# Kernel optimization log

Hardware: AMD Instinct MI355X
Metric: run time of the kernel (lower is better)

The kernel has to match this reference:

```python
import jax, jax.numpy as jnp
import numpy as np

N = 100000
E = 1600000
IN_DIM, HID, OUT = 128, 64, 16
NUM_CLASSES = 2
BN_EPS = 1e-5


def setup_inputs() -> dict:
    key = jax.random.key(0)
    ks = jax.random.split(key, 12)
    s = lambda fan_in: 1.0 / np.sqrt(fan_in)
    inp = {
        'x': jax.random.normal(ks[0], (N, IN_DIM), jnp.float32),
        'src': jax.random.randint(ks[1], (E,), 0, N, jnp.int32),
        'dst': jax.random.randint(ks[2], (E,), 0, N, jnp.int32),
        # SAGEConv1: lin_l (neighbors, bias) + lin_r (root, no bias)
        'W1l': jax.random.uniform(ks[3], (HID, IN_DIM), jnp.float32, -s(IN_DIM), s(IN_DIM)),
        'b1l': jnp.zeros((HID,), jnp.float32),
        'W1r': jax.random.uniform(ks[4], (HID, IN_DIM), jnp.float32, -s(IN_DIM), s(IN_DIM)),
        # BatchNorm1d(hidden)
        'gamma': jnp.ones((HID,), jnp.float32),
        'beta': jnp.zeros((HID,), jnp.float32),
        # SAGEConv2
        'W2l': jax.random.uniform(ks[5], (OUT, HID), jnp.float32, -s(HID), s(HID)),
        'b2l': jnp.zeros((OUT,), jnp.float32),
        'W2r': jax.random.uniform(ks[6], (OUT, HID), jnp.float32, -s(HID), s(HID)),
        # classifier Linear(emb_dim=16, 2)
        'Wc': jax.random.uniform(ks[7], (NUM_CLASSES, OUT), jnp.float32, -s(OUT), s(OUT)),
        'bc': jax.random.uniform(ks[8], (NUM_CLASSES,), jnp.float32, -s(OUT), s(OUT)),
    }
    return inp


def _sage_conv(x, src, dst, Wl, bl, Wr, deg_inv):
    # mean-aggregate neighbor features at dst, then linear; plus root transform
    agg = jax.ops.segment_sum(x[src], dst, num_segments=N) * deg_inv  # [N, F]
    return agg @ Wl.T + bl + x @ Wr.T


def _batchnorm_train(h, gamma, beta):
    mu = jnp.mean(h, axis=0)
    var = jnp.mean((h - mu) ** 2, axis=0)  # biased, as torch BN uses for normalization
    return (h - mu) * jax.lax.rsqrt(var + BN_EPS) * gamma + beta


def reference(x, src, dst, W1l, b1l, W1r, gamma, beta, W2l, b2l, W2r, Wc, bc):
    deg = jax.ops.segment_sum(jnp.ones((E,), x.dtype), dst, num_segments=N)
    deg_inv = (1.0 / jnp.maximum(deg, 1.0))[:, None]
    h = _sage_conv(x, src, dst, W1l, b1l, W1r, deg_inv)      # [N, HID]
    h = jax.nn.relu(_batchnorm_train(h, gamma, beta))
    emb = _sage_conv(h, src, dst, W2l, b2l, W2r, deg_inv)    # [N, OUT]
    logits = emb @ Wc.T + bc                                 # [N, 2]
    return (logits, emb)
```

## Files before the change

### kernel.cpp

```cpp
#include <hip/hip_runtime.h>

#define NN 100000
#define NB ((NN + 255) / 256)

__device__ __forceinline__ unsigned short f2bf(float x) {
    unsigned u = __float_as_uint(x);
    u += 0x7fff + ((u >> 16) & 1);
    return (unsigned short)(u >> 16);
}
__device__ __forceinline__ float bf2f(unsigned short h) {
    return __uint_as_float(((unsigned)h) << 16);
}

template<bool BF16>
__device__ __forceinline__ void gemm32x64(const float* __restrict__ x,
        const float* __restrict__ W, void* __restrict__ out,
        int rb, int tid, float (*lw)[68], float (*lx)[68]) {
    const int row0 = rb * 32;
    const int cg = tid & 15, rl = tid >> 4;
    float acc[2][4] = {{0.f,0.f,0.f,0.f},{0.f,0.f,0.f,0.f}};
    for (int kt = 0; kt < 2; ++kt) {
        if (kt) __syncthreads();
        for (int idx = tid; idx < 4096; idx += 256) {
            int j = idx >> 6, k = idx & 63;
            lw[k][j] = W[j * 128 + kt * 64 + k];
        }
        #pragma unroll
        for (int i = 0; i < 2; ++i) {
            int f4 = i * 256 + tid;
            int r = f4 >> 4, k4 = (f4 & 15) << 2;
            int grow = row0 + r;
            float4 vv = make_float4(0.f, 0.f, 0.f, 0.f);
            if (grow < NN) vv = *(const float4*)(x + (size_t)grow * 128 + kt * 64 + k4);
            *(float4*)(&lx[r][k4]) = vv;
        }
        __syncthreads();
        #pragma unroll
        for (int p = 0; p < 2; ++p) {
            int r = p * 16 + rl;
            #pragma unroll 8
            for (int k = 0; k < 64; ++k) {
                float xv = lx[r][k];
                float4 wv = *(const float4*)(&lw[k][cg << 2]);
                acc[p][0] = fmaf(xv, wv.x, acc[p][0]);
                acc[p][1] = fmaf(xv, wv.y, acc[p][1]);
                acc[p][2] = fmaf(xv, wv.z, acc[p][2]);
                acc[p][3] = fmaf(xv, wv.w, acc[p][3]);
            }
        }
    }
    #pragma unroll
    for (int p = 0; p < 2; ++p) {
        int grow = row0 + p * 16 + rl;
        if (grow < NN) {
            if (BF16) {
                ushort4 o;
                o.x = f2bf(acc[p][0]); o.y = f2bf(acc[p][1]);
                o.z = f2bf(acc[p][2]); o.w = f2bf(acc[p][3]);
                *(ushort4*)((unsigned short*)out + (size_t)grow * 64 + (cg << 2)) = o;
            } else {
                *(float4*)((float*)out + (size_t)grow * 64 + (cg << 2)) =
                    make_float4(acc[p][0], acc[p][1], acc[p][2], acc[p][3]);
            }
        }
    }
}

__global__ __launch_bounds__(256) void k_fusedA(const float* __restrict__ x,
        const float* __restrict__ W1l, const int* __restrict__ dst,
        int* __restrict__ deg, unsigned short* __restrict__ y1, int E) {
    __shared__ float lw[64][68];
    __shared__ float lx[32][68];
    const int tid = threadIdx.x;
    const int u = blockIdx.x >> 4, v = blockIdx.x & 15;
    if (v < 8) {
        const int base = (u * 8 + v) * 512;
        #pragma unroll
        for (int i = 0; i < 2; ++i) {
            int e = base + i * 256 + tid;
            if (e < E) atomicAdd(&deg[dst[e]], 1);
        }
        return;
    }
    const int rb = u * 8 + (v - 8);
    if (rb >= 3125) return;
    gemm32x64<true>(x, W1l, y1, rb, tid, lw, lx);
}

__global__ __launch_bounds__(256) void k_fusedB(const float* __restrict__ x,
        const float* __restrict__ W1r, const int* __restrict__ src,
        const int* __restrict__ dst, int* __restrict__ cursor,
        int* __restrict__ eidx, float* __restrict__ h, int E) {
    __shared__ float lw[64][68];
    __shared__ float lx[32][68];
    const int tid = threadIdx.x;
    const int u = blockIdx.x >> 4, v = blockIdx.x & 15;
    if (v < 8) {
        const int base = u * 4096;
        const int lo = v * 12500, hi = lo + 12500;
        #pragma unroll 4
        for (int i = 0; i < 16; ++i) {
            int e = base + i * 256 + tid;
            if (e < E) {
                int d = dst[e];
                if (d >= lo && d < hi) {
                    int pos = atomicAdd(&cursor[d], 1);
                    eidx[pos] = src[e];
                }
            }
        }
        return;
    }
    const int rb = u * 8 + (v - 8);
    if (rb >= 3125) return;
    gemm32x64<false>(x, W1r, h, rb, tid, lw, lx);
}

__global__ __launch_bounds__(256) void k_scanA(const int* __restrict__ deg,
                                               int* __restrict__ rowptr,
                                               int* __restrict__ bsum) {
    const int tid = threadIdx.x;
    const int i = blockIdx.x * 256 + tid;
    int v = (i < NN) ? deg[i] : 0;
    const int lane = tid & 63, w = tid >> 6;
    int inc = v;
    #pragma unroll
    for (int d = 1; d < 64; d <<= 1) {
        int t = __shfl_up(inc, d, 64);
        if (lane >= d) inc += t;
    }
    __shared__ int wsum[4];
    if (lane == 63) wsum[w] = inc;
    __syncthreads();
    int wo = 0;
    for (int k = 0; k < w; ++k) wo += wsum[k];
    if (i < NN) rowptr[i] = wo + inc - v;
    if (tid == 255) bsum[blockIdx.x] = wo + inc;
}

__global__ __launch_bounds__(512) void k_scanB(int* __restrict__ bsum,
                                               int* __restrict__ rowptr, int E) {
    const int tid = threadIdx.x;
    int v = (tid < NB) ? bsum[tid] : 0;
    const int lane = tid & 63, w = tid >> 6;
    int inc = v;
    #pragma unroll
    for (int d = 1; d < 64; d <<= 1) {
        int t = __shfl_up(inc, d, 64);
        if (lane >= d) inc += t;
    }
    __shared__ int wsum[8];
    if (lane == 63) wsum[w] = inc;
    __syncthreads();
    int wo = 0;
    for (int k = 0; k < w; ++k) wo += wsum[k];
    if (tid < NB) bsum[tid] = wo + inc - v;
    if (tid == 0) rowptr[NN] = E;
}

__global__ void k_finish(int* __restrict__ rowptr, const int* __restrict__ bsum,
                         const int* __restrict__ deg, int* __restrict__ cursor,
                         float* __restrict__ deg_inv) {
    int i = blockIdx.x * 256 + threadIdx.x;
    if (i < NN) {
        int rp = rowptr[i] + bsum[i >> 8];
        rowptr[i] = rp;
        cursor[i] = rp;
        deg_inv[i] = 1.0f / fmaxf((float)deg[i], 1.0f);
    }
}

__global__ __launch_bounds__(256) void k_gather1(const unsigned short* __restrict__ y1,
        const int* __restrict__ rowptr, const int* __restrict__ eidx,
        const float* __restrict__ b1l,
        const float* __restrict__ deg_inv, float* __restrict__ h,
        float* __restrict__ stats) {
    const int tid = threadIdx.x;
    const int f = tid & 63, w = tid >> 6;
    const float bias = b1l[f];
    float a1 = 0.f, a2 = 0.f;
    for (int n = blockIdx.x * 4 + w; n < NN; n += gridDim.x * 4) {
        int beg = rowptr[n], end = rowptr[n + 1];
        float s0 = 0.f, s1 = 0.f, s2 = 0.f, s3 = 0.f;
        int j = beg;
        for (; j + 3 < end; j += 4) {
            int i0 = eidx[j], i1 = eidx[j + 1], i2 = eidx[j + 2], i3 = eidx[j + 3];
            s0 += bf2f(y1[(size_t)i0 * 64 + f]);
            s1 += bf2f(y1[(size_t)i1 * 64 + f]);
            s2 += bf2f(y1[(size_t)i2 * 64 + f]);
            s3 += bf2f(y1[(size_t)i3 * 64 + f]);
        }
        for (; j < end; ++j) s0 += bf2f(y1[(size_t)eidx[j] * 64 + f]);
        size_t off = (size_t)n * 64 + f;
        float hv = fmaf((s0 + s1) + (s2 + s3), deg_inv[n], h[off] + bias);
        h[off] = hv;
        a1 += hv; a2 = fmaf(hv, hv, a2);
    }
    __shared__ float sA[4][64], sB[4][64];
    sA[w][f] = a1; sB[w][f] = a2;
    __syncthreads();
    if (w == 0) {
        atomicAdd(&stats[f],      sA[0][f] + sA[1][f] + sA[2][f] + sA[3][f]);
        atomicAdd(&stats[64 + f], sB[0][f] + sB[1][f] + sB[2][f] + sB[3][f]);
    }
}

__global__ __launch_bounds__(256) void k_gemm2(const float* __restrict__ h,
        const float* __restrict__ W2l, const float* __restrict__ W2r,
        const float* __restrict__ stats, const float* __restrict__ gamma,
        const float* __restrict__ beta,
        unsigned short* __restrict__ y2, float* __restrict__ hr2) {
    __shared__ float lh[64][68];
    __shared__ float lw[64][36];
    __shared__ float lsc[64], lsh[64];
    const int tid = threadIdx.x;
    if (tid < 64) {
        float mu = stats[tid] * (1.0f / NN);
        float var = stats[64 + tid] * (1.0f / NN) - mu * mu;
        float sc = gamma[tid] * rsqrtf(var + 1e-5f);
        lsc[tid] = sc;
        lsh[tid] = beta[tid] - mu * sc;
    }
    for (int idx = tid; idx < 32 * 64; idx += 256) {
        int j = idx >> 6, k = idx & 63;
        lw[k][j] = (j < 16) ? W2l[idx] : W2r[idx - 1024];
    }
    __syncthreads();
    const int row0 = blockIdx.x * 64;
    for (int i = 0; i < 4; ++i) {
        int f4 = i * 256 + tid;
        int r = f4 >> 4;
        int k4 = (f4 & 15) << 2;
        int grow = row0 + r;
        float4 v = make_float4(0.f, 0.f, 0.f, 0.f);
        if (grow < NN) v = *(const float4*)(h + (size_t)grow * 64 + k4);
        float4 sc = *(const float4*)(&lsc[k4]);
        float4 sh = *(const float4*)(&lsh[k4]);
        float4 o;
        o.x = fmaxf(fmaf(v.x, sc.x, sh.x), 0.f);
        o.y = fmaxf(fmaf(v.y, sc.y, sh.y), 0.f);
        o.z = fmaxf(fmaf(v.z, sc.z, sh.z), 0.f);
        o.w = fmaxf(fmaf(v.w, sc.w, sh.w), 0.f);
        *(float4*)(&lh[r][k4]) = o;
    }
    __syncthreads();
    const int cg = tid & 7;
    const int rl = tid >> 3;
    #pragma unroll
    for (int p = 0; p < 2; ++p) {
        int r = p * 32 + rl;
        int grow = row0 + r;
        float ax = 0.f, ay = 0.f, az = 0.f, aw = 0.f;
        #pragma unroll
        for (int k = 0; k < 64; ++k) {
            float hv = lh[r][k];
            float4 wv = *(const float4*)(&lw[k][cg << 2]);
            ax = fmaf(hv, wv.x, ax); ay = fmaf(hv, wv.y, ay);
            az = fmaf(hv, wv.z, az); aw = fmaf(hv, wv.w, aw);
        }
        if (grow < NN) {
            int c = cg << 2;
            if (c < 16) {
                ushort4 o;
                o.x = f2bf(ax); o.y = f2bf(ay); o.z = f2bf(az); o.w = f2bf(aw);
                *(ushort4*)(y2 + (size_t)grow * 16 + c) = o;
            } else {
                *(float4*)(hr2 + (size_t)grow * 16 + (c - 16)) = make_float4(ax, ay, az, aw);
            }
        }
    }
}

__global__ __launch_bounds__(256) void k_gather2(const unsigned short* __restrict__ y2,
        const int* __restrict__ rowptr, const int* __restrict__ eidx,
        const float* __restrict__ hr2, const float* __restrict__ b2l,
        const float* __restrict__ deg_inv, const float* __restrict__ Wc,
        const float* __restrict__ bc, float* __restrict__ out) {
    const int tid = threadIdx.x;
    const int f = tid & 15, g = tid >> 4;
    const float wc0 = Wc[f], wc1 = Wc[16 + f];
    const float bias = b2l[f];
    for (int n = blockIdx.x * 16 + g; n < NN; n += gridDim.x * 16) {
        int beg = rowptr[n], end = rowptr[n + 1];
        float s0 = 0.f, s1 = 0.f, s2 = 0.f, s3 = 0.f;
        int j = beg;
        for (; j + 3 < end; j += 4) {
            int i0 = eidx[j], i1 = eidx[j + 1], i2 = eidx[j + 2], i3 = eidx[j + 3];
            s0 += bf2f(y2[(size_t)i0 * 16 + f]);
            s1 += bf2f(y2[(size_t)i1 * 16 + f]);
            s2 += bf2f(y2[(size_t)i2 * 16 + f]);
            s3 += bf2f(y2[(size_t)i3 * 16 + f]);
        }
        for (; j < end; ++j) s0 += bf2f(y2[(size_t)eidx[j] * 16 + f]);
        float e = fmaf((s0 + s1) + (s2 + s3), deg_inv[n], hr2[(size_t)n * 16 + f] + bias);
        out[(size_t)(2 * NN) + (size_t)n * 16 + f] = e;
        float l0 = e * wc0, l1 = e * wc1;
        #pragma unroll
        for (int m = 1; m < 16; m <<= 1) {
            l0 += __shfl_xor(l0, m, 64);
            l1 += __shfl_xor(l1, m, 64);
        }
        if (f == 0) {
            out[(size_t)n * 2]     = l0 + bc[0];
            out[(size_t)n * 2 + 1] = l1 + bc[1];
        }
    }
}

extern "C" void kernel_launch(void* const* d_in, const int* in_sizes, int n_in,
                              void* d_out, int out_size, void* d_ws, size_t ws_size,
                              hipStream_t stream) {
    const float* x     = (const float*)d_in[0];
    const int*   src   = (const int*)d_in[1];
    const int*   dst   = (const int*)d_in[2];
    const float* W1l   = (const float*)d_in[3];
    const float* b1l   = (const float*)d_in[4];
    const float* W1r   = (const float*)d_in[5];
    const float* gamma = (const float*)d_in[6];
    const float* beta  = (const float*)d_in[7];
    const float* W2l   = (const float*)d_in[8];
    const float* b2l   = (const float*)d_in[9];
    const float* W2r   = (const float*)d_in[10];
    const float* Wc    = (const float*)d_in[11];
    const float* bc    = (const float*)d_in[12];
    const int E = in_sizes[1];

    float* ws      = (float*)d_ws;
    int*   rowptr  = (int*)ws;
    float* deg_inv = ws + 100352;
    float* stats   = ws + 200704;
    int*   deg_i   = (int*)(ws + 200960);
    int*   cursor  = (int*)(ws + 301312);
    int*   eidx    = (int*)(ws + 401664);
    float* y1reg   = ws + 401664 + (size_t)E;
    float* h       = y1reg + (size_t)NN * 64;
    unsigned short* y1 = (unsigned short*)y1reg;
    int*   bsum    = eidx;
    unsigned short* y2 = (unsigned short*)y1reg;
    float* hr2     = y1reg + (size_t)NN * 8;
    float* out     = (float*)d_out;

    hipMemsetAsync(deg_i, 0, NN * sizeof(int), stream);
    hipMemsetAsync(stats, 0, 256 * sizeof(float), stream);

    k_fusedA<<<6256, 256, 0, stream>>>(x, W1l, dst, deg_i, y1, E);

    k_scanA<<<NB, 256, 0, stream>>>(deg_i, rowptr, bsum);
    k_scanB<<<1, 512, 0, stream>>>(bsum, rowptr, E);
    k_finish<<<NB, 256, 0, stream>>>(rowptr, bsum, deg_i, cursor, deg_inv);

    k_fusedB<<<6256, 256, 0, stream>>>(x, W1r, src, dst, cursor, eidx, h, E);

    k_gather1<<<4096, 256, 0, stream>>>(y1, rowptr, eidx, b1l, deg_inv, h, stats);

    k_gemm2<<<(NN + 63) / 64, 256, 0, stream>>>(h, W2l, W2r, stats, gamma, beta, y2, hr2);

    k_gather2<<<2048, 256, 0, stream>>>(y2, rowptr, eidx, hr2, b2l, deg_inv, Wc, bc, out);
}
```

Before: 448.3 us.

## Fuse both layer-1 GEMMs into one dual-weight tile pass split across kernels

Replaces the two separate 32x64 GEMMs (W1l in k_fusedA, W1r in k_fusedB) with a single 64-row tile kernel that computes both projections from one load of x, then splits the row tiles between the two fused kernels. Each x row is read once instead of twice. Each thread now computes a 4x4 register tile per weight. The edge-processing blocks each handle four times as many edges, which cuts the grid to 1568 blocks. The trade-off is higher register and LDS use (three 64x68 tiles), which lowers occupancy, and coarser edge work per block.

```diff
diff --git a/kernel.cpp b/kernel.cpp
--- a/kernel.cpp
+++ b/kernel.cpp
@@ -2,6 +2,8 @@
 
 #define NN 100000
 #define NB ((NN + 255) / 256)
+#define NT 1563
+#define SPLIT 782
 
 __device__ __forceinline__ unsigned short f2bf(float x) {
     unsigned u = __float_as_uint(x);
@@ -12,94 +14,106 @@
     return __uint_as_float(((unsigned)h) << 16);
 }
 
-template<bool BF16>
-__device__ __forceinline__ void gemm32x64(const float* __restrict__ x,
-        const float* __restrict__ W, void* __restrict__ out,
-        int rb, int tid, float (*lw)[68], float (*lx)[68]) {
-    const int row0 = rb * 32;
-    const int cg = tid & 15, rl = tid >> 4;
-    float acc[2][4] = {{0.f,0.f,0.f,0.f},{0.f,0.f,0.f,0.f}};
+__device__ __forceinline__ void gemm_dual(const float* __restrict__ x,
+        const float* __restrict__ Wl, const float* __restrict__ Wr,
+        unsigned short* __restrict__ y1, float* __restrict__ h,
+        int rb, int tid, float (*lx)[68], float (*lwl)[68], float (*lwr)[68]) {
+    const int row0 = rb * 64;
+    const int cg = tid & 15, rq = tid >> 4;
+    float accL[4][4] = {{0.f}}, accR[4][4] = {{0.f}};
     for (int kt = 0; kt < 2; ++kt) {
         if (kt) __syncthreads();
-        for (int idx = tid; idx < 4096; idx += 256) {
-            int j = idx >> 6, k = idx & 63;
-            lw[k][j] = W[j * 128 + kt * 64 + k];
-        }
-        #pragma unroll
-        for (int i = 0; i < 2; ++i) {
-            int f4 = i * 256 + tid;
-            int r = f4 >> 4, k4 = (f4 & 15) << 2;
+        #pragma unroll
+        for (int i = 0; i < 4; ++i) {
+            int idx = i * 256 + tid;
+            int r = idx >> 4, k4 = (idx & 15) << 2;
             int grow = row0 + r;
-            float4 vv = make_float4(0.f, 0.f, 0.f, 0.f);
-            if (grow < NN) vv = *(const float4*)(x + (size_t)grow * 128 + kt * 64 + k4);
-            *(float4*)(&lx[r][k4]) = vv;
+            float4 v = make_float4(0.f, 0.f, 0.f, 0.f);
+            if (grow < NN) v = *(const float4*)(x + (size_t)grow * 128 + kt * 64 + k4);
+            *(float4*)(&lx[r][k4]) = v;
+        }
+        #pragma unroll
+        for (int i = 0; i < 4; ++i) {
+            int idx = i * 256 + tid;
+            int j = idx & 63, k4 = (idx >> 6) << 2;
+            float4 a = *(const float4*)(Wl + (size_t)j * 128 + kt * 64 + k4);
+            lwl[k4 + 0][j] = a.x; lwl[k4 + 1][j] = a.y;
+            lwl[k4 + 2][j] = a.z; lwl[k4 + 3][j] = a.w;
+            float4 b = *(const float4*)(Wr + (size_t)j * 128 + kt * 64 + k4);
+            lwr[k4 + 0][j] = b.x; lwr[k4 + 1][j] = b.y;
+            lwr[k4 + 2][j] = b.z; lwr[k4 + 3][j] = b.w;
         }
         __syncthreads();
-        #pragma unroll
-        for (int p = 0; p < 2; ++p) {
-            int r = p * 16 + rl;
-            #pragma unroll 8
-            for (int k = 0; k < 64; ++k) {
-                float xv = lx[r][k];
-                float4 wv = *(const float4*)(&lw[k][cg << 2]);
-                acc[p][0] = fmaf(xv, wv.x, acc[p][0]);
-                acc[p][1] = fmaf(xv, wv.y, acc[p][1]);
-                acc[p][2] = fmaf(xv, wv.z, acc[p][2]);
-                acc[p][3] = fmaf(xv, wv.w, acc[p][3]);
+        #pragma unroll 4
+        for (int k = 0; k < 64; ++k) {
+            float4 wl = *(const float4*)(&lwl[k][cg << 2]);
+            float4 wr = *(const float4*)(&lwr[k][cg << 2]);
+            #pragma unroll
+            for (int i = 0; i < 4; ++i) {
+                float xv = lx[rq * 4 + i][k];
+                accL[i][0] = fmaf(xv, wl.x, accL[i][0]);
+                accL[i][1] = fmaf(xv, wl.y, accL[i][1]);
+                accL[i][2] = fmaf(xv, wl.z, accL[i][2]);
+                accL[i][3] = fmaf(xv, wl.w, accL[i][3]);
+                accR[i][0] = fmaf(xv, wr.x, accR[i][0]);
+                accR[i][1] = fmaf(xv, wr.y, accR[i][1]);
+                accR[i][2] = fmaf(xv, wr.z, accR[i][2]);
+                accR[i][3] = fmaf(xv, wr.w, accR[i][3]);
             }
         }
     }
     #pragma unroll
-    for (int p = 0; p < 2; ++p) {
-        int grow = row0 + p * 16 + rl;
+    for (int i = 0; i < 4; ++i) {
+        int grow = row0 + rq * 4 + i;
         if (grow < NN) {
-            if (BF16) {
-                ushort4 o;
-                o.x = f2bf(acc[p][0]); o.y = f2bf(acc[p][1]);
-                o.z = f2bf(acc[p][2]); o.w = f2bf(acc[p][3]);
-                *(ushort4*)((unsigned short*)out + (size_t)grow * 64 + (cg << 2)) = o;
-            } else {
-                *(float4*)((float*)out + (size_t)grow * 64 + (cg << 2)) =
-                    make_float4(acc[p][0], acc[p][1], acc[p][2], acc[p][3]);
-            }
+            ushort4 o;
+            o.x = f2bf(accL[i][0]); o.y = f2bf(accL[i][1]);
+            o.z = f2bf(accL[i][2]); o.w = f2bf(accL[i][3]);
+            *(ushort4*)(y1 + (size_t)grow * 64 + (cg << 2)) = o;
+            *(float4*)(h + (size_t)grow * 64 + (cg << 2)) =
+                make_float4(accR[i][0], accR[i][1], accR[i][2], accR[i][3]);
         }
     }
 }
 
 __global__ __launch_bounds__(256) void k_fusedA(const float* __restrict__ x,
-        const float* __restrict__ W1l, const int* __restrict__ dst,
-        int* __restrict__ deg, unsigned short* __restrict__ y1, int E) {
-    __shared__ float lw[64][68];
-    __shared__ float lx[32][68];
+        const float* __restrict__ W1l, const float* __restrict__ W1r,
+        const int* __restrict__ dst, int* __restrict__ deg,
+        unsigned short* __restrict__ y1, float* __restrict__ h, int E) {
+    __shared__ float lx[64][68];
+    __shared__ float lwl[64][68];
+    __shared__ float lwr[64][68];
     const int tid = threadIdx.x;
     const int u = blockIdx.x >> 4, v = blockIdx.x & 15;
     if (v < 8) {
-        const int base = (u * 8 + v) * 512;
-        #pragma unroll
-        for (int i = 0; i < 2; ++i) {
+        const int base = (u * 8 + v) * 2048;
+        #pragma unroll
+        for (int i = 0; i < 8; ++i) {
             int e = base + i * 256 + tid;
             if (e < E) atomicAdd(&deg[dst[e]], 1);
         }
         return;
     }
     const int rb = u * 8 + (v - 8);
-    if (rb >= 3125) return;
-    gemm32x64<true>(x, W1l, y1, rb, tid, lw, lx);
+    if (rb >= SPLIT) return;
+    gemm_dual(x, W1l, W1r, y1, h, rb, tid, lx, lwl, lwr);
 }
 
 __global__ __launch_bounds__(256) void k_fusedB(const float* __restrict__ x,
-        const float* __restrict__ W1r, const int* __restrict__ src,
-        const int* __restrict__ dst, int* __restrict__ cursor,
-        int* __restrict__ eidx, float* __restrict__ h, int E) {
-    __shared__ float lw[64][68];
-    __shared__ float lx[32][68];
+        const float* __restrict__ W1l, const float* __restrict__ W1r,
+        const int* __restrict__ src, const int* __restrict__ dst,
+        int* __restrict__ cursor, int* __restrict__ eidx,
+        unsigned short* __restrict__ y1, float* __restrict__ h, int E) {
+    __shared__ float lx[64][68];
+    __shared__ float lwl[64][68];
+    __shared__ float lwr[64][68];
     const int tid = threadIdx.x;
     const int u = blockIdx.x >> 4, v = blockIdx.x & 15;
     if (v < 8) {
-        const int base = u * 4096;
+        const int base = u * 16384;
         const int lo = v * 12500, hi = lo + 12500;
         #pragma unroll 4
-        for (int i = 0; i < 16; ++i) {
+        for (int i = 0; i < 64; ++i) {
             int e = base + i * 256 + tid;
             if (e < E) {
                 int d = dst[e];
@@ -111,9 +125,9 @@
         }
         return;
     }
-    const int rb = u * 8 + (v - 8);
-    if (rb >= 3125) return;
-    gemm32x64<false>(x, W1r, h, rb, tid, lw, lx);
+    const int rb = SPLIT + u * 8 + (v - 8);
+    if (rb >= NT) return;
+    gemm_dual(x, W1l, W1r, y1, h, rb, tid, lx, lwl, lwr);
 }
 
 __global__ __launch_bounds__(256) void k_scanA(const int* __restrict__ deg,
@@ -343,13 +357,13 @@
     hipMemsetAsync(deg_i, 0, NN * sizeof(int), stream);
     hipMemsetAsync(stats, 0, 256 * sizeof(float), stream);
 
-    k_fusedA<<<6256, 256, 0, stream>>>(x, W1l, dst, deg_i, y1, E);
+    k_fusedA<<<1568, 256, 0, stream>>>(x, W1l, W1r, dst, deg_i, y1, h, E);
 
     k_scanA<<<NB, 256, 0, stream>>>(deg_i, rowptr, bsum);
     k_scanB<<<1, 512, 0, stream>>>(bsum, rowptr, E);
     k_finish<<<NB, 256, 0, stream>>>(rowptr, bsum, deg_i, cursor, deg_inv);
 
-    k_fusedB<<<6256, 256, 0, stream>>>(x, W1r, src, dst, cursor, eidx, h, E);
+    k_fusedB<<<1568, 256, 0, stream>>>(x, W1l, W1r, src, dst, cursor, eidx, y1, h, E);
 
     k_gather1<<<4096, 256, 0, stream>>>(y1, rowptr, eidx, b1l, deg_inv, h, stats);
 
```

New measurement: 493.9 us. +10.2%, slower.
